# Kernel optimization log

Hardware: AMD Instinct MI355X
Metric: run time of the kernel (lower is better)

## Reference

```python
import jax, jax.numpy as jnp
import numpy as np

B, IN, H, NOPT = 16384, 4096, 128, 64
GAIN = 0.5  # default control_gains value in the module


def gru_cell(x, h, Wih, Whh, bih, bhh):
    # torch GRU single step; gate order r, z, n
    gi = x @ Wih + bih          # [B, 3H]
    gh = h @ Whh + bhh          # [B, 3H]
    ir, iz, inn = jnp.split(gi, 3, axis=-1)
    hr, hz, hn = jnp.split(gh, 3, axis=-1)
    r = jax.nn.sigmoid(ir + hr)
    z = jax.nn.sigmoid(iz + hz)
    n = jnp.tanh(inn + r * hn)
    return (1.0 - z) * n + z * h


def setup_inputs() -> dict:
    key = jax.random.key(0)
    ks = jax.random.split(key, 12)
    s = lambda k, shape: (jax.random.normal(k, shape, jnp.float32) * 0.05)
    return {
        "obs": jax.random.normal(ks[0], (B, IN), jnp.float32),
        "chosen_option": jax.random.randint(ks[1], (B,), 0, NOPT),
        "h0": jnp.zeros((B, H), jnp.float32),
        "h1": jnp.zeros((B, H), jnp.float32),
        "Wa": s(ks[2], (IN, H)), "ba": jnp.zeros((H,), jnp.float32),
        "Wih0": s(ks[3], (H, 3 * H)), "Whh0": s(ks[4], (H, 3 * H)),
        "bih0": jnp.zeros((3 * H,), jnp.float32), "bhh0": jnp.zeros((3 * H,), jnp.float32),
        "Wih1": s(ks[5], (2 * H, 3 * H)), "Whh1": s(ks[6], (H, 3 * H)),
        "bih1": jnp.zeros((3 * H,), jnp.float32), "bhh1": jnp.zeros((3 * H,), jnp.float32),
        "Wv0": s(ks[7], (H, NOPT)), "bv0": jnp.zeros((NOPT,), jnp.float32),
        "Wv1": s(ks[8], (H, NOPT)), "bv1": jnp.zeros((NOPT,), jnp.float32),
        "Wt0": s(ks[9], (H, NOPT)), "bt0": jnp.zeros((NOPT,), jnp.float32),
    }


def reference(obs, chosen_option, h0, h1, Wa, ba, Wih0, Whh0, bih0, bhh0,
              Wih1, Whh1, bih1, bhh1, Wv0, bv0, Wv1, bv1, Wt0, bt0):
    # attention: tanh(Linear(obs))
    attn = jnp.tanh(obs @ Wa + ba)                       # [B, H]
    # layer 0: GRU on attn
    h0n = gru_cell(attn, h0, Wih0, Whh0, bih0, bhh0)     # [B, H]
    hc0 = (h0n - 0.5) * GAIN + 0.5                       # gain contrast
    v0 = hc0 @ Wv0 + bv0                                 # [B, NOPT]
    term = jax.nn.sigmoid(hc0 @ Wt0 + bt0)               # [B, NOPT]
    term_p = jnp.take_along_axis(term, chosen_option[:, None], axis=1)  # [B, 1]
    # layer 1: GRU on cat(attn, own hidden)
    x1 = jnp.concatenate([attn, h1], axis=-1)            # [B, 2H]
    h1n = gru_cell(x1, h1, Wih1, Whh1, bih1, bhh1)       # [B, H]
    hc1 = (h1n - 0.5) * GAIN + 0.5
    v1 = hc1 @ Wv1 + bv1                                 # [B, NOPT]
    return v0, term_p, v1, h0n, h1n
```

## Files before the change

kernel.cpp:

```cpp
#include <hip/hip_runtime.h>
#include <hip/hip_bf16.h>
#include <stdint.h>


typedef __attribute__((ext_vector_type(8))) short bf16x8;
typedef __attribute__((ext_vector_type(4))) float f32x4;
typedef __attribute__((ext_vector_type(8))) float f32x8;

#define INDIM 4096
#define H 128
#define NOPT 64

#define WS_WAT    0u
#define WS_WIH0T  524288u
#define WS_WHH0T  573440u
#define WS_WIH1T  622592u
#define WS_WHH1T  720896u
#define WS_WV0T   770048u
#define WS_WV1T   778240u
#define WS_WT0T   786432u

#define OUT_V0    0u
#define OUT_TERMP 1048576u
#define OUT_V1    1064960u
#define OUT_H0N   2113536u
#define OUT_H1N   4210688u

static __device__ __forceinline__ uint16_t f2bf(float f) {
  __hip_bfloat16 h = __float2bfloat16(f);
  return __builtin_bit_cast(uint16_t, h);
}
static __device__ __forceinline__ float sigm(float x) { return 1.0f / (1.0f + __expf(-x)); }
static __device__ __forceinline__ float fast_tanh(float x) {
  float e = __expf(2.0f * x);
  return 1.0f - 2.0f / (e + 1.0f);
}
static __device__ __forceinline__ f32x4 mfma16(bf16x8 a, bf16x8 b, f32x4 c) {
  return __builtin_amdgcn_mfma_f32_16x16x32_bf16(a, b, c, 0, 0, 0);
}
static __device__ __forceinline__ bf16x8 cvt8(f32x8 v) {
  bf16x8 r;
#pragma unroll
  for (int j = 0; j < 8; ++j) r[j] = (short)f2bf(v[j]);
  return r;
}

__global__ void k_transpose(const float* __restrict__ Wa,
                            const float* __restrict__ Wih0,
                            const float* __restrict__ Whh0,
                            const float* __restrict__ Wih1,
                            const float* __restrict__ Whh1,
                            const float* __restrict__ Wv0,
                            const float* __restrict__ Wv1,
                            const float* __restrict__ Wt0,
                            uint16_t* __restrict__ ws) {
  int blk = blockIdx.x;
  const float* in; uint16_t* out; int ksh; int N; int base;
  if (blk < 2048)      { in = Wa;   out = ws + WS_WAT;   ksh = 12; N = 128; base = 0; }
  else if (blk < 2240) { in = Wih0; out = ws + WS_WIH0T; ksh = 7;  N = 384; base = 2048; }
  else if (blk < 2432) { in = Whh0; out = ws + WS_WHH0T; ksh = 7;  N = 384; base = 2240; }
  else if (blk < 2816) { in = Wih1; out = ws + WS_WIH1T; ksh = 8;  N = 384; base = 2432; }
  else if (blk < 3008) { in = Whh1; out = ws + WS_WHH1T; ksh = 7;  N = 384; base = 2816; }
  else if (blk < 3040) { in = Wv0;  out = ws + WS_WV0T;  ksh = 7;  N = 64;  base = 3008; }
  else if (blk < 3072) { in = Wv1;  out = ws + WS_WV1T;  ksh = 7;  N = 64;  base = 3040; }
  else                 { in = Wt0;  out = ws + WS_WT0T;  ksh = 7;  N = 64;  base = 3072; }
  int e = (blk - base) * 256 + (int)threadIdx.x;
  int n = e >> ksh;
  int k = e & ((1 << ksh) - 1);
  out[e] = f2bf(in[(size_t)k * N + n]);
}

__launch_bounds__(256, 4)
__global__ void k_fused(const float* __restrict__ obs,
                        const uint16_t* __restrict__ ws,
                        const float* __restrict__ ba,
                        const float* __restrict__ h0,
                        const float* __restrict__ bih0,
                        const float* __restrict__ bhh0,
                        const float* __restrict__ bv0,
                        const float* __restrict__ bt0,
                        const int* __restrict__ chosen,
                        const float* __restrict__ h1,
                        const float* __restrict__ bih1,
                        const float* __restrict__ bhh1,
                        const float* __restrict__ bv1,
                        float* __restrict__ out) {
  __shared__ uint16_t sX[16 * 16 * 8];
  __shared__ uint16_t sC[16 * 16 * 8];
  const uint16_t* WaT   = ws + WS_WAT;
  const uint16_t* Wih0T = ws + WS_WIH0T;
  const uint16_t* Whh0T = ws + WS_WHH0T;
  const uint16_t* Wih1T = ws + WS_WIH1T;
  const uint16_t* Whh1T = ws + WS_WHH1T;
  const uint16_t* Wv0T  = ws + WS_WV0T;
  const uint16_t* Wv1T  = ws + WS_WV1T;
  const uint16_t* Wt0T  = ws + WS_WT0T;
  const int t = threadIdx.x, w = t >> 6, lane = t & 63;
  const int l15 = lane & 15, quad = lane >> 4;
  const int row0 = blockIdx.x * 16;
  const int nbA = 2 * w;

  f32x4 acc0 = {}, acc1 = {};
  {
    const float*    arow  = obs + (size_t)(row0 + l15) * INDIM + quad * 8;
    const uint16_t* brow0 = WaT + (size_t)(nbA * 16 + l15) * INDIM + quad * 8;
    const uint16_t* brow1 = brow0 + (size_t)16 * INDIM;
#pragma unroll 2
    for (int kt = 0; kt < 64; ++kt) {
      const int k0 = kt * 64;
      f32x8 av0 = *(const f32x8*)(arow + k0);
      f32x8 av1 = *(const f32x8*)(arow + k0 + 32);
      bf16x8 b00 = *(const bf16x8*)(brow0 + k0);
      bf16x8 b01 = *(const bf16x8*)(brow0 + k0 + 32);
      bf16x8 b10 = *(const bf16x8*)(brow1 + k0);
      bf16x8 b11 = *(const bf16x8*)(brow1 + k0 + 32);
      bf16x8 a0 = cvt8(av0);
      bf16x8 a1 = cvt8(av1);
      acc0 = mfma16(a0, b00, acc0);
      acc0 = mfma16(a1, b01, acc0);
      acc1 = mfma16(a0, b10, acc1);
      acc1 = mfma16(a1, b11, acc1);
    }
  }
#pragma unroll
  for (int nbl = 0; nbl < 2; ++nbl) {
    const f32x4 A = nbl ? acc1 : acc0;
    const int col = (nbA + nbl) * 16 + l15;
    const float bav = ba[col];
    const int kb = col >> 3;
#pragma unroll
    for (int i = 0; i < 4; ++i) {
      const int r = quad * 4 + i;
      sX[(r * 16 + (kb ^ r)) * 8 + (col & 7)] = f2bf(fast_tanh(A[i] + bav));
    }
  }
  __syncthreads();

  bf16x8 ax[4], ah[4];
  {
    const float* hrow = h0 + (size_t)(row0 + l15) * H + quad * 8;
#pragma unroll
    for (int ks = 0; ks < 4; ++ks) {
      const int kb = ks * 4 + quad;
      ax[ks] = *(const bf16x8*)&sX[(l15 * 16 + (kb ^ l15)) * 8];
      ah[ks] = cvt8(*(const f32x8*)(hrow + ks * 32));
    }
  }
#pragma unroll
  for (int nbl = 0; nbl < 2; ++nbl) {
    const int nrow = (nbA + nbl) * 16 + l15;
    f32x4 air = {}, ahr = {}, aiz = {}, ahz = {}, ain = {}, ahn = {};
#pragma unroll
    for (int ks = 0; ks < 4; ++ks) {
      const int k = ks * 32 + quad * 8;
      bf16x8 b;
      b = *(const bf16x8*)(Wih0T + (size_t)(nrow      ) * H + k); air = mfma16(ax[ks], b, air);
      b = *(const bf16x8*)(Wih0T + (size_t)(nrow + 128) * H + k); aiz = mfma16(ax[ks], b, aiz);
      b = *(const bf16x8*)(Wih0T + (size_t)(nrow + 256) * H + k); ain = mfma16(ax[ks], b, ain);
      b = *(const bf16x8*)(Whh0T + (size_t)(nrow      ) * H + k); ahr = mfma16(ah[ks], b, ahr);
      b = *(const bf16x8*)(Whh0T + (size_t)(nrow + 128) * H + k); ahz = mfma16(ah[ks], b, ahz);
      b = *(const bf16x8*)(Whh0T + (size_t)(nrow + 256) * H + k); ahn = mfma16(ah[ks], b, ahn);
    }
    const int col = nrow;
    const float b_ir = bih0[col],       b_hr = bhh0[col];
    const float b_iz = bih0[col + 128], b_hz = bhh0[col + 128];
    const float b_in = bih0[col + 256], b_hn = bhh0[col + 256];
    const int kb = col >> 3;
#pragma unroll
    for (int i = 0; i < 4; ++i) {
      const int r = quad * 4 + i;
      const int grow = row0 + r;
      const float rr = sigm(air[i] + ahr[i] + b_ir + b_hr);
      const float zz = sigm(aiz[i] + ahz[i] + b_iz + b_hz);
      const float nn = fast_tanh(ain[i] + b_in + rr * (ahn[i] + b_hn));
      const float hv = h0[(size_t)grow * H + col];
      const float hnew = (1.0f - zz) * nn + zz * hv;
      out[OUT_H0N + (size_t)grow * H + col] = hnew;
      sC[(r * 16 + (kb ^ r)) * 8 + (col & 7)] = f2bf(0.5f * hnew + 0.25f);
    }
  }
  __syncthreads();

  {
    int ch[4];
#pragma unroll
    for (int i = 0; i < 4; ++i) ch[i] = chosen[row0 + quad * 4 + i];
    bf16x8 ac[4];
#pragma unroll
    for (int ks = 0; ks < 4; ++ks) {
      const int kb = ks * 4 + quad;
      ac[ks] = *(const bf16x8*)&sC[(l15 * 16 + (kb ^ l15)) * 8];
    }
    f32x4 av = {}, at = {};
    const int nrow = w * 16 + l15;
#pragma unroll
    for (int ks = 0; ks < 4; ++ks) {
      const int k = ks * 32 + quad * 8;
      bf16x8 b;
      b = *(const bf16x8*)(Wv0T + (size_t)nrow * H + k); av = mfma16(ac[ks], b, av);
      b = *(const bf16x8*)(Wt0T + (size_t)nrow * H + k); at = mfma16(ac[ks], b, at);
    }
    const int col = nrow;
    const float bvv = bv0[col], btv = bt0[col];
#pragma unroll
    for (int i = 0; i < 4; ++i) {
      const int grow = row0 + quad * 4 + i;
      out[OUT_V0 + (size_t)grow * NOPT + col] = av[i] + bvv;
      if (ch[i] == col)
        out[OUT_TERMP + grow] = sigm(at[i] + btv);
    }
  }
  __syncthreads();

  bf16x8 ah1[4];
  {
    const float* hrow = h1 + (size_t)(row0 + l15) * H + quad * 8;
#pragma unroll
    for (int ks = 0; ks < 4; ++ks)
      ah1[ks] = cvt8(*(const f32x8*)(hrow + ks * 32));
  }
#pragma unroll
  for (int nbl = 0; nbl < 2; ++nbl) {
    const int nrow = (nbA + nbl) * 16 + l15;
    f32x4 air = {}, ahr = {}, aiz = {}, ahz = {}, ain = {}, ahn = {};
#pragma unroll
    for (int ks = 0; ks < 8; ++ks) {
      const int k = ks * 32 + quad * 8;
      const bf16x8 a = (ks < 4) ? ax[ks] : ah1[ks - 4];
      bf16x8 b;
      b = *(const bf16x8*)(Wih1T + (size_t)(nrow      ) * 256 + k); air = mfma16(a, b, air);
      b = *(const bf16x8*)(Wih1T + (size_t)(nrow + 128) * 256 + k); aiz = mfma16(a, b, aiz);
      b = *(const bf16x8*)(Wih1T + (size_t)(nrow + 256) * 256 + k); ain = mfma16(a, b, ain);
    }
#pragma unroll
    for (int ks = 0; ks < 4; ++ks) {
      const int k = ks * 32 + quad * 8;
      bf16x8 b;
      b = *(const bf16x8*)(Whh1T + (size_t)(nrow      ) * H + k); ahr = mfma16(ah1[ks], b, ahr);
      b = *(const bf16x8*)(Whh1T + (size_t)(nrow + 128) * H + k); ahz = mfma16(ah1[ks], b, ahz);
      b = *(const bf16x8*)(Whh1T + (size_t)(nrow + 256) * H + k); ahn = mfma16(ah1[ks], b, ahn);
    }
    const int col = nrow;
    const float b_ir = bih1[col],       b_hr = bhh1[col];
    const float b_iz = bih1[col + 128], b_hz = bhh1[col + 128];
    const float b_in = bih1[col + 256], b_hn = bhh1[col + 256];
    const int kb = col >> 3;
#pragma unroll
    for (int i = 0; i < 4; ++i) {
      const int r = quad * 4 + i;
      const int grow = row0 + r;
      const float rr = sigm(air[i] + ahr[i] + b_ir + b_hr);
      const float zz = sigm(aiz[i] + ahz[i] + b_iz + b_hz);
      const float nn = fast_tanh(ain[i] + b_in + rr * (ahn[i] + b_hn));
      const float hv = h1[(size_t)grow * H + col];
      const float hnew = (1.0f - zz) * nn + zz * hv;
      out[OUT_H1N + (size_t)grow * H + col] = hnew;
      sC[(r * 16 + (kb ^ r)) * 8 + (col & 7)] = f2bf(0.5f * hnew + 0.25f);
    }
  }
  __syncthreads();

  {
    bf16x8 ac[4];
#pragma unroll
    for (int ks = 0; ks < 4; ++ks) {
      const int kb = ks * 4 + quad;
      ac[ks] = *(const bf16x8*)&sC[(l15 * 16 + (kb ^ l15)) * 8];
    }
    f32x4 av = {};
    const int nrow = w * 16 + l15;
#pragma unroll
    for (int ks = 0; ks < 4; ++ks) {
      const int k = ks * 32 + quad * 8;
      bf16x8 b = *(const bf16x8*)(Wv1T + (size_t)nrow * H + k);
      av = mfma16(ac[ks], b, av);
    }
    const int col = nrow;
    const float bvv = bv1[col];
#pragma unroll
    for (int i = 0; i < 4; ++i) {
      const int grow = row0 + quad * 4 + i;
      out[OUT_V1 + (size_t)grow * NOPT + col] = av[i] + bvv;
    }
  }
}

extern "C" void kernel_launch(void* const* d_in, const int* in_sizes, int n_in,
                              void* d_out, int out_size, void* d_ws, size_t ws_size,
                              hipStream_t stream) {
  (void)in_sizes; (void)n_in; (void)out_size; (void)ws_size;
  const float* obs    = (const float*)d_in[0];
  const int*   chosen = (const int*)d_in[1];
  const float* h0     = (const float*)d_in[2];
  const float* h1     = (const float*)d_in[3];
  const float* Wa     = (const float*)d_in[4];
  const float* ba     = (const float*)d_in[5];
  const float* Wih0   = (const float*)d_in[6];
  const float* Whh0   = (const float*)d_in[7];
  const float* bih0   = (const float*)d_in[8];
  const float* bhh0   = (const float*)d_in[9];
  const float* Wih1   = (const float*)d_in[10];
  const float* Whh1   = (const float*)d_in[11];
  const float* bih1   = (const float*)d_in[12];
  const float* bhh1   = (const float*)d_in[13];
  const float* Wv0    = (const float*)d_in[14];
  const float* bv0    = (const float*)d_in[15];
  const float* Wv1    = (const float*)d_in[16];
  const float* bv1    = (const float*)d_in[17];
  const float* Wt0    = (const float*)d_in[18];
  const float* bt0    = (const float*)d_in[19];
  uint16_t* ws  = (uint16_t*)d_ws;
  float*    out = (float*)d_out;

  hipLaunchKernelGGL(k_transpose, dim3(3104), dim3(256), 0, stream,
                     Wa, Wih0, Whh0, Wih1, Whh1, Wv0, Wv1, Wt0, ws);
  hipLaunchKernelGGL(k_fused, dim3(1024), dim3(256), 0, stream,
                     obs, ws, ba, h0, bih0, bhh0, bv0, bt0, chosen,
                     h1, bih1, bhh1, bv1, out);
}
```

Before: 620.5 us.

## Stage obs tile in LDS once per block and tile weight transpose

The first GEMM previously had every wave load and convert the same 16 fp32 obs rows, so each block read obs four times. Now each thread loads one 8-float chunk per 128-wide K step, converts it to bf16 once into a double-buffered swizzled LDS tile, and all waves read MFMA fragments from LDS. This adds a barrier per K step. The weight transpose kernel now uses 32x32 shared-memory tiles so both reads and writes are coalesced, replacing the strided per-element gather.

```diff
diff --git a/kernel.cpp b/kernel.cpp
--- a/kernel.cpp
+++ b/kernel.cpp
@@ -54,20 +54,34 @@
                             const float* __restrict__ Wv1,
                             const float* __restrict__ Wt0,
                             uint16_t* __restrict__ ws) {
+  __shared__ float sT[32][34];
   int blk = blockIdx.x;
-  const float* in; uint16_t* out; int ksh; int N; int base;
-  if (blk < 2048)      { in = Wa;   out = ws + WS_WAT;   ksh = 12; N = 128; base = 0; }
-  else if (blk < 2240) { in = Wih0; out = ws + WS_WIH0T; ksh = 7;  N = 384; base = 2048; }
-  else if (blk < 2432) { in = Whh0; out = ws + WS_WHH0T; ksh = 7;  N = 384; base = 2240; }
-  else if (blk < 2816) { in = Wih1; out = ws + WS_WIH1T; ksh = 8;  N = 384; base = 2432; }
-  else if (blk < 3008) { in = Whh1; out = ws + WS_WHH1T; ksh = 7;  N = 384; base = 2816; }
-  else if (blk < 3040) { in = Wv0;  out = ws + WS_WV0T;  ksh = 7;  N = 64;  base = 3008; }
-  else if (blk < 3072) { in = Wv1;  out = ws + WS_WV1T;  ksh = 7;  N = 64;  base = 3040; }
-  else                 { in = Wt0;  out = ws + WS_WT0T;  ksh = 7;  N = 64;  base = 3072; }
-  int e = (blk - base) * 256 + (int)threadIdx.x;
-  int n = e >> ksh;
-  int k = e & ((1 << ksh) - 1);
-  out[e] = f2bf(in[(size_t)k * N + n]);
+  const float* in; uint16_t* out; int K; int N; int base;
+  if (blk < 512)      { in = Wa;   out = ws + WS_WAT;   K = 4096; N = 128; base = 0; }
+  else if (blk < 560) { in = Wih0; out = ws + WS_WIH0T; K = 128;  N = 384; base = 512; }
+  else if (blk < 608) { in = Whh0; out = ws + WS_WHH0T; K = 128;  N = 384; base = 560; }
+  else if (blk < 704) { in = Wih1; out = ws + WS_WIH1T; K = 256;  N = 384; base = 608; }
+  else if (blk < 752) { in = Whh1; out = ws + WS_WHH1T; K = 128;  N = 384; base = 704; }
+  else if (blk < 760) { in = Wv0;  out = ws + WS_WV0T;  K = 128;  N = 64;  base = 752; }
+  else if (blk < 768) { in = Wv1;  out = ws + WS_WV1T;  K = 128;  N = 64;  base = 760; }
+  else                { in = Wt0;  out = ws + WS_WT0T;  K = 128;  N = 64;  base = 768; }
+  const int tix = blk - base;
+  const int nTK = K >> 5;
+  const int kt = tix & (nTK - 1);
+  const int nt = tix / nTK;
+  const int k0 = kt * 32, n0 = nt * 32;
+  const int t = threadIdx.x;
+#pragma unroll
+  for (int i = 0; i < 4; ++i) {
+    int e = i * 256 + t, kk = e >> 5, nn = e & 31;
+    sT[kk][nn] = in[(size_t)(k0 + kk) * N + n0 + nn];
+  }
+  __syncthreads();
+#pragma unroll
+  for (int i = 0; i < 4; ++i) {
+    int e = i * 256 + t, nn = e >> 5, kk = e & 31;
+    out[(size_t)(n0 + nn) * K + k0 + kk] = f2bf(sT[kk][nn]);
+  }
 }
 
 __launch_bounds__(256, 4)
@@ -85,6 +99,7 @@
                         const float* __restrict__ bhh1,
                         const float* __restrict__ bv1,
                         float* __restrict__ out) {
+  __shared__ uint16_t sObs[2][16 * 16 * 8];
   __shared__ uint16_t sX[16 * 16 * 8];
   __shared__ uint16_t sC[16 * 16 * 8];
   const uint16_t* WaT   = ws + WS_WAT;
@@ -102,24 +117,30 @@
 
   f32x4 acc0 = {}, acc1 = {};
   {
-    const float*    arow  = obs + (size_t)(row0 + l15) * INDIM + quad * 8;
+    const int r16 = t >> 4;
+    const int kb16 = t & 15;
+    const float* aptr = obs + (size_t)(row0 + r16) * INDIM + kb16 * 8;
+    const int wslot = (r16 * 16 + (kb16 ^ r16)) * 8;
     const uint16_t* brow0 = WaT + (size_t)(nbA * 16 + l15) * INDIM + quad * 8;
     const uint16_t* brow1 = brow0 + (size_t)16 * INDIM;
-#pragma unroll 2
-    for (int kt = 0; kt < 64; ++kt) {
-      const int k0 = kt * 64;
-      f32x8 av0 = *(const f32x8*)(arow + k0);
-      f32x8 av1 = *(const f32x8*)(arow + k0 + 32);
-      bf16x8 b00 = *(const bf16x8*)(brow0 + k0);
-      bf16x8 b01 = *(const bf16x8*)(brow0 + k0 + 32);
-      bf16x8 b10 = *(const bf16x8*)(brow1 + k0);
-      bf16x8 b11 = *(const bf16x8*)(brow1 + k0 + 32);
-      bf16x8 a0 = cvt8(av0);
-      bf16x8 a1 = cvt8(av1);
-      acc0 = mfma16(a0, b00, acc0);
-      acc0 = mfma16(a1, b01, acc0);
-      acc1 = mfma16(a0, b10, acc1);
-      acc1 = mfma16(a1, b11, acc1);
+    f32x8 stg = *(const f32x8*)(aptr);
+    for (int kt = 0; kt < 32; ++kt) {
+      *(bf16x8*)&sObs[kt & 1][wslot] = cvt8(stg);
+      if (kt < 31) stg = *(const f32x8*)(aptr + (size_t)(kt + 1) * 128);
+      bf16x8 b[8];
+      const int kO = kt * 128;
+#pragma unroll
+      for (int s = 0; s < 4; ++s) {
+        b[s]     = *(const bf16x8*)(brow0 + kO + s * 32);
+        b[4 + s] = *(const bf16x8*)(brow1 + kO + s * 32);
+      }
+      __syncthreads();
+#pragma unroll
+      for (int s = 0; s < 4; ++s) {
+        bf16x8 afr = *(const bf16x8*)&sObs[kt & 1][(l15 * 16 + ((s * 4 + quad) ^ l15)) * 8];
+        acc0 = mfma16(afr, b[s], acc0);
+        acc1 = mfma16(afr, b[4 + s], acc1);
+      }
     }
   }
 #pragma unroll
@@ -312,7 +333,7 @@
   uint16_t* ws  = (uint16_t*)d_ws;
   float*    out = (float*)d_out;
 
-  hipLaunchKernelGGL(k_transpose, dim3(3104), dim3(256), 0, stream,
+  hipLaunchKernelGGL(k_transpose, dim3(776), dim3(256), 0, stream,
                      Wa, Wih0, Whh0, Wih1, Whh1, Wv0, Wv1, Wt0, ws);
   hipLaunchKernelGGL(k_fused, dim3(1024), dim3(256), 0, stream,
                      obs, ws, ba, h0, bih0, bhh0, bv0, bt0, chosen,
```

After: 521.1 us. 1.19x faster.
